# Performance work log

Hardware: AMD Instinct MI355X
Metric: run time of the kernel (lower is better)

The kernel has to match this reference:

```python
import jax, jax.numpy as jnp
import numpy as np

D_MODEL = 1024
N_HEADS = 16
D_K = D_MODEL // N_HEADS
D_FF = 4096
EPS = 1e-5


def _layernorm(x, g, b):
    mu = jnp.mean(x, axis=-1, keepdims=True)
    var = jnp.var(x, axis=-1, keepdims=True)
    return (x - mu) * jax.lax.rsqrt(var + EPS) * g + b


def setup_inputs() -> dict:
    key = jax.random.key(0)
    ks = jax.random.split(key, 12)
    s = 0.02
    x = jax.random.normal(ks[0], (2, 2048, D_MODEL), dtype=jnp.float32)
    # Linear weights stored [in, out] so y = x @ W + b
    wq = jax.random.normal(ks[1], (D_MODEL, D_MODEL), dtype=jnp.float32) * s
    wk = jax.random.normal(ks[2], (D_MODEL, D_MODEL), dtype=jnp.float32) * s
    wv = jax.random.normal(ks[3], (D_MODEL, D_MODEL), dtype=jnp.float32) * s
    wo = jax.random.normal(ks[4], (D_MODEL, D_MODEL), dtype=jnp.float32) * s
    bq = jnp.zeros((D_MODEL,), jnp.float32)
    bk = jnp.zeros((D_MODEL,), jnp.float32)
    bv = jnp.zeros((D_MODEL,), jnp.float32)
    bo = jnp.zeros((D_MODEL,), jnp.float32)
    ln1_g = jnp.ones((D_MODEL,), jnp.float32)
    ln1_b = jnp.zeros((D_MODEL,), jnp.float32)
    ln2_g = jnp.ones((D_MODEL,), jnp.float32)
    ln2_b = jnp.zeros((D_MODEL,), jnp.float32)
    w1 = jax.random.normal(ks[5], (D_MODEL, D_FF), dtype=jnp.float32) * s
    b1 = jnp.zeros((D_FF,), jnp.float32)
    w2 = jax.random.normal(ks[6], (D_FF, D_MODEL), dtype=jnp.float32) * s
    b2 = jnp.zeros((D_MODEL,), jnp.float32)
    return {"x": x, "wq": wq, "bq": bq, "wk": wk, "bk": bk, "wv": wv, "bv": bv,
            "wo": wo, "bo": bo, "ln1_g": ln1_g, "ln1_b": ln1_b,
            "ln2_g": ln2_g, "ln2_b": ln2_b, "w1": w1, "b1": b1, "w2": w2, "b2": b2}


def reference(x, wq, bq, wk, bk, wv, bv, wo, bo, ln1_g, ln1_b, ln2_g, ln2_b, w1, b1, w2, b2):
    B, S, _ = x.shape
    res = x
    # project and split heads: [B, S, H, Dk]
    q = (x @ wq + bq).reshape(B, S, N_HEADS, D_K)
    k = (x @ wk + bk).reshape(B, S, N_HEADS, D_K)
    v = (x @ wv + bv).reshape(B, S, N_HEADS, D_K)
    # full score matrix [B, H, Sq, Sk] (faithful to unfused original)
    scores = jnp.einsum('bqhd,bkhd->bhqk', q, k) / jnp.sqrt(jnp.float32(D_K))
    weights = jax.nn.softmax(scores, axis=-1)
    attn = jnp.einsum('bhqk,bkhd->bqhd', weights, v).reshape(B, S, D_MODEL)
    x = _layernorm(res + attn @ wo + bo, ln1_g, ln1_b)
    res = x
    h = jax.nn.relu(x @ w1 + b1)
    x = _layernorm(res + h @ w2 + b2, ln2_g, ln2_b)
    return x
```

## Files before the change

kernel.cpp:

```cpp
#include <hip/hip_runtime.h>
#include <hip/hip_bf16.h>
#include <stdint.h>


typedef __hip_bfloat16 bf16;
typedef short bf16x8 __attribute__((ext_vector_type(8)));
typedef float f32x4 __attribute__((ext_vector_type(4)));

#if __has_builtin(__builtin_amdgcn_exp2f)
#define EXP2F(x) __builtin_amdgcn_exp2f(x)
#else
#define EXP2F(x) exp2f(x)
#endif

__device__ __forceinline__ float bf2f_lo(unsigned u) { return __uint_as_float(u << 16); }
__device__ __forceinline__ float bf2f_hi(unsigned u) { return __uint_as_float(u & 0xffff0000u); }
__device__ __forceinline__ ushort f2bf(float f) {
  union { bf16 h; ushort u; } c; c.h = __float2bfloat16(f); return c.u;
}
__device__ __forceinline__ uint pk_bf16(float a, float b) {
  union { __hip_bfloat162 h2; uint u; } c;
  c.h2 = __float22bfloat162_rn(make_float2(a, b));
  return c.u;
}
__device__ __forceinline__ bool is_f32(const uint* probe) { return probe[0] == 0x3F800000u; }
__device__ __forceinline__ float ld_param(const void* p, size_t i, bool f32) {
  return f32 ? ((const float*)p)[i] : __bfloat162float(((const bf16*)p)[i]);
}

__device__ __forceinline__ void barrier_raw() {
  asm volatile("" ::: "memory");
  __builtin_amdgcn_s_barrier();
  asm volatile("" ::: "memory");
}
__device__ __forceinline__ void lgkm0() {
  asm volatile("s_waitcnt lgkmcnt(0)" ::: "memory");
}
__device__ __forceinline__ void glds16(const ushort* g, ushort* l) {
  __builtin_amdgcn_global_load_lds(
      (const __attribute__((address_space(1))) void*)g,
      (__attribute__((address_space(3))) void*)l, 16, 0, 0);
}

#define MFMA16(MH, NH)                                                        \
  do {                                                                        \
    _Pragma("unroll") for (int c_ = 0; c_ < 2; ++c_)                          \
    _Pragma("unroll") for (int fi_ = 0; fi_ < 4; ++fi_)                       \
    _Pragma("unroll") for (int gi_ = 0; gi_ < 2; ++gi_)                       \
      acc[(MH) * 4 + fi_][(NH) * 2 + gi_] =                                   \
          __builtin_amdgcn_mfma_f32_16x16x32_bf16(                            \
              areg[fi_][c_], breg[(NH) * 2 + gi_][c_],                        \
              acc[(MH) * 4 + fi_][(NH) * 2 + gi_], 0, 0, 0);                  \
  } while (0)

__device__ __forceinline__ void gemm256_body(
    const ushort* __restrict__ A, const ushort* __restrict__ BT,
    const void* __restrict__ bias, const void* __restrict__ res,
    void* __restrict__ C, int N_, int K_, int bm, int bn,
    int kb, int ke, int mode, const uint* probe) {
  __shared__ ushort As[2][16384];
  __shared__ ushort Bs[2][16384];

  const int tid = threadIdx.x;
  const int wave = tid >> 6;
  const int lane = tid & 63;
  const int wm = wave >> 2;
  const int wn = wave & 3;
  const int m16 = lane & 15;
  const int quad = lane >> 4;
  const int nt = (ke - kb) >> 6;

  const int srow = lane >> 2;
  const int skc = ((lane & 3) * 8) ^ (((lane >> 5) & 1) << 4);
  const ushort* pA = A + (size_t)(bm * 256 + wave * 16 + srow) * K_ + kb + skc;
  const ushort* pB = BT + (size_t)(bn * 256 + wave * 16 + srow) * K_ + kb + skc;
  const size_t hstep = (size_t)128 * K_;
  ushort* dA = &As[0][0] + wave * 1024;
  ushort* dB = &Bs[0][0] + wave * 1024;

  auto stageA = [&](int b, int half, int t) {
    const ushort* g = pA + (size_t)half * hstep + t * 64;
    ushort* d = dA + b * 16384 + half * 8192;
    glds16(g, d);
    glds16(g + 32, d + 512);
  };
  auto stageB = [&](int b, int half, int t) {
    const ushort* g = pB + (size_t)half * hstep + t * 64;
    ushort* d = dB + b * 16384 + half * 8192;
    glds16(g, d);
    glds16(g + 32, d + 512);
  };

  const int fr_off = m16 * 32 + ((quad * 8) ^ (((m16 >> 3) & 1) << 4));
  const ushort* rA = &As[0][0] + fr_off;
  const ushort* rB = &Bs[0][0] + fr_off;
  auto ldA = [&](int b, int f, int c) {
    return *(const bf16x8*)(rA + b * 16384 +
                            ((f >> 2) * 8 + wm * 4 + (f & 3)) * 1024 + c * 512);
  };
  auto ldB = [&](int b, int g, int c) {
    return *(const bf16x8*)(rB + b * 16384 +
                            ((g >> 1) * 8 + wn * 2 + (g & 1)) * 1024 + c * 512);
  };

  f32x4 acc[8][4];
#pragma unroll
  for (int f = 0; f < 8; ++f)
#pragma unroll
    for (int g = 0; g < 4; ++g) acc[f][g] = (f32x4){0.f, 0.f, 0.f, 0.f};
  bf16x8 areg[4][2], breg[4][2];

  stageA(0, 0, 0); stageB(0, 0, 0); stageA(0, 1, 0); stageB(0, 1, 0);
  if (nt > 1) { stageA(1, 0, 1); stageB(1, 0, 1); }
  asm volatile("s_waitcnt vmcnt(4)" ::: "memory");
  barrier_raw();

  for (int t = 0; t < nt; ++t) {
    const int b = t & 1, bo = b ^ 1;
#pragma unroll
    for (int fi = 0; fi < 4; ++fi) { areg[fi][0] = ldA(b, fi, 0); areg[fi][1] = ldA(b, fi, 1); }
#pragma unroll
    for (int gi = 0; gi < 2; ++gi) { breg[gi][0] = ldB(b, gi, 0); breg[gi][1] = ldB(b, gi, 1); }
    if (t + 1 < nt) stageA(bo, 1, t + 1);
    barrier_raw(); lgkm0();
    __builtin_amdgcn_s_setprio(1); MFMA16(0, 0); __builtin_amdgcn_s_setprio(0);
    barrier_raw();
#pragma unroll
    for (int gi = 2; gi < 4; ++gi) { breg[gi][0] = ldB(b, gi, 0); breg[gi][1] = ldB(b, gi, 1); }
    if (t + 1 < nt) stageB(bo, 1, t + 1);
    barrier_raw(); lgkm0();
    __builtin_amdgcn_s_setprio(1); MFMA16(0, 1); __builtin_amdgcn_s_setprio(0);
    barrier_raw();
#pragma unroll
    for (int fi = 0; fi < 4; ++fi) { areg[fi][0] = ldA(b, fi + 4, 0); areg[fi][1] = ldA(b, fi + 4, 1); }
    if (t + 2 < nt) stageA(b, 0, t + 2);
    barrier_raw(); lgkm0();
    __builtin_amdgcn_s_setprio(1); MFMA16(1, 0); __builtin_amdgcn_s_setprio(0);
    barrier_raw();
    if (t + 2 < nt) stageB(b, 0, t + 2);
    barrier_raw(); lgkm0();
    __builtin_amdgcn_s_setprio(1); MFMA16(1, 1); __builtin_amdgcn_s_setprio(0);
    if (t + 2 < nt) asm volatile("s_waitcnt vmcnt(4)" ::: "memory");
    else            asm volatile("s_waitcnt vmcnt(0)" ::: "memory");
    barrier_raw();
  }

  const bool F32 = is_f32(probe);
#pragma unroll
  for (int g = 0; g < 4; ++g) {
    const int col = bn * 256 + (g >> 1) * 128 + wn * 32 + (g & 1) * 16 + m16;
    const float bv = (mode >= 3) ? 0.f : ld_param(bias, col, F32);
#pragma unroll
    for (int f = 0; f < 8; ++f) {
      const int rowb = bm * 256 + (f >> 2) * 128 + wm * 64 + (f & 3) * 16 + quad * 4;
#pragma unroll
      for (int r = 0; r < 4; ++r) {
        const int row = rowb + r;
        float v = acc[f][g][r] + bv;
        if (mode == 1) v = fmaxf(v, 0.f);
        if (mode == 2) v += __bfloat162float(((const bf16*)res)[(size_t)row * N_ + col]);
        if (mode == 2 || mode == 3) ((float*)C)[(size_t)row * N_ + col] = v;
        else ((bf16*)C)[(size_t)row * N_ + col] = __float2bfloat16(v);
      }
    }
  }
}

__global__ __launch_bounds__(512, 2) void gemm256_qkv(
    const ushort* A, const ushort* BT0, const ushort* BT1, const ushort* BT2,
    const void* b0, const void* b1, const void* b2,
    bf16* C0, bf16* C1, bf16* C2, const uint* probe) {
  const int sel = blockIdx.y >> 2, bn = blockIdx.y & 3;
  const ushort* BT = sel == 0 ? BT0 : (sel == 1 ? BT1 : BT2);
  const void* bb = sel == 0 ? b0 : (sel == 1 ? b1 : b2);
  bf16* C = sel == 0 ? C0 : (sel == 1 ? C1 : C2);
  gemm256_body(A, BT, bb, nullptr, C, 1024, 1024, blockIdx.x, bn, 0, 1024, 0, probe);
}
__global__ __launch_bounds__(512, 2) void gemm256_ffn1(
    const ushort* A, const ushort* BT, const void* bias, bf16* C, const uint* probe) {
  gemm256_body(A, BT, bias, nullptr, C, 4096, 1024,
               blockIdx.x, blockIdx.y, 0, 1024, 1, probe);
}
__global__ __launch_bounds__(512, 2) void gemm256_ffn2_sk4(
    const ushort* A, const ushort* BT,
    bf16* P0, bf16* P1, bf16* P2, bf16* P3, const uint* probe) {
  const int kz = blockIdx.z;
  bf16* C = kz == 0 ? P0 : kz == 1 ? P1 : kz == 2 ? P2 : P3;
  gemm256_body(A, BT, nullptr, nullptr, C, 1024, 4096, blockIdx.x, blockIdx.y,
               kz * 1024, kz * 1024 + 1024, 4, probe);
}

template <bool A_EXT, bool RES_EXT>
__device__ __forceinline__ void gemm_body(
    const void* __restrict__ Av, const ushort* __restrict__ BT,
    const void* __restrict__ bias, const void* __restrict__ res,
    void* __restrict__ C, int N_, int K_, int bm, int bn,
    int kb, int ke, int mode, const uint* probe) {
  __shared__ ushort Asm_[128 * 32];
  __shared__ ushort Bsm_[128 * 32];

  const bool F32 = is_f32(probe);
  const bool AF = A_EXT && F32;

  const int tid = threadIdx.x;
  const int wave = tid >> 6;
  const int lane = tid & 63;
  const int wm = wave & 1, wn = wave >> 1;

  const int r0 = tid >> 2;
  const int c0 = (tid & 3) * 8;
  const int dA0 = r0 * 32 + c0;
  const int dA1 = dA0 + 64 * 32;

  const size_t aRow0 = (size_t)(bm * 128 + r0) * K_;
  const size_t aRow1 = aRow0 + (size_t)64 * K_;
  const ushort* pB0 = BT + (size_t)(bn * 128 + r0) * K_ + c0;
  const ushort* pB1 = pB0 + (size_t)64 * K_;

  auto ld4 = [&](int kk, uint4& A0, uint4& A1, uint4& B0, uint4& B1) {
    if (AF) {
      const float* Af = (const float*)Av;
      const float4 f0 = *(const float4*)(Af + aRow0 + kk + c0);
      const float4 f1 = *(const float4*)(Af + aRow0 + kk + c0 + 4);
      const float4 g0 = *(const float4*)(Af + aRow1 + kk + c0);
      const float4 g1 = *(const float4*)(Af + aRow1 + kk + c0 + 4);
      A0.x = pk_bf16(f0.x, f0.y); A0.y = pk_bf16(f0.z, f0.w);
      A0.z = pk_bf16(f1.x, f1.y); A0.w = pk_bf16(f1.z, f1.w);
      A1.x = pk_bf16(g0.x, g0.y); A1.y = pk_bf16(g0.z, g0.w);
      A1.z = pk_bf16(g1.x, g1.y); A1.w = pk_bf16(g1.z, g1.w);
    } else {
      const ushort* Ab = (const ushort*)Av;
      A0 = *(const uint4*)(Ab + aRow0 + kk + c0);
      A1 = *(const uint4*)(Ab + aRow1 + kk + c0);
    }
    B0 = *(const uint4*)(pB0 + kk);
    B1 = *(const uint4*)(pB1 + kk);
  };

  f32x4 zero = {0.f, 0.f, 0.f, 0.f};
  f32x4 acc[4][4];
#pragma unroll
  for (int i = 0; i < 4; ++i)
#pragma unroll
    for (int j = 0; j < 4; ++j) acc[i][j] = zero;

  const int m16 = lane & 15;
  const int quad = lane >> 4;
  const int koff = quad * 8;

  uint4 a0, a1, b0, b1;
  ld4(kb, a0, a1, b0, b1);

  for (int k0 = kb; k0 < ke; k0 += 32) {
    __syncthreads();
    *(uint4*)&Asm_[dA0] = a0;
    *(uint4*)&Asm_[dA1] = a1;
    *(uint4*)&Bsm_[dA0] = b0;
    *(uint4*)&Bsm_[dA1] = b1;
    __syncthreads();

    if (k0 + 32 < ke) ld4(k0 + 32, a0, a1, b0, b1);

    bf16x8 af[4], bfr[4];
#pragma unroll
    for (int i = 0; i < 4; ++i)
      af[i] = *(const bf16x8*)&Asm_[(wm * 64 + i * 16 + m16) * 32 + koff];
#pragma unroll
    for (int j = 0; j < 4; ++j)
      bfr[j] = *(const bf16x8*)&Bsm_[(wn * 64 + j * 16 + m16) * 32 + koff];
#pragma unroll
    for (int i = 0; i < 4; ++i)
#pragma unroll
      for (int j = 0; j < 4; ++j)
        acc[i][j] = __builtin_amdgcn_mfma_f32_16x16x32_bf16(af[i], bfr[j], acc[i][j], 0, 0, 0);
  }

  const int row0 = bm * 128 + wm * 64;
  const int col0 = bn * 128 + wn * 64;
#pragma unroll
  for (int j = 0; j < 4; ++j) {
    const int col = col0 + j * 16 + m16;
    const float bv = (mode == 3) ? 0.f : ld_param(bias, col, F32);
#pragma unroll
    for (int i = 0; i < 4; ++i) {
#pragma unroll
      for (int r = 0; r < 4; ++r) {
        const int row = row0 + i * 16 + quad * 4 + r;
        float v = acc[i][j][r] + bv;
        if (mode == 1) v = fmaxf(v, 0.f);
        if (mode == 2) v += ld_param(res, (size_t)row * N_ + col, RES_EXT && F32);
        if (mode >= 2) ((float*)C)[(size_t)row * N_ + col] = v;
        else ((bf16*)C)[(size_t)row * N_ + col] = __float2bfloat16(v);
      }
    }
  }
}

__global__ __launch_bounds__(256) void gemm_wo_sk(
    const ushort* A, const ushort* BT, const void* bias, const void* res,
    float* C0, float* C1, const uint* probe) {
  const int kz = blockIdx.z;
  gemm_body<false, true>(A, BT, bias, res, kz ? C1 : C0, 1024, 1024,
                         blockIdx.x, blockIdx.y, kz * 512, kz * 512 + 512,
                         kz ? 3 : 2, probe);
}

__global__ __launch_bounds__(256) void transpose_all(
    const void* W0, const void* W1, const void* W2, const void* W3,
    const void* W4, const void* W5, const void* X6,
    ushort* D0, ushort* D1, ushort* D2, ushort* D3, ushort* D4, ushort* D5,
    ushort* D6, const uint* probe) {
  const int z = blockIdx.z;
  if (z == 6) {
    const bool F32 = is_f32(probe);
    const size_t i =
        ((size_t)(blockIdx.y * 128 + blockIdx.x) * 256 + threadIdx.x) * 4;
    if (F32) {
      const float4 a = *(const float4*)((const float*)X6 + i);
      uint2 o; o.x = pk_bf16(a.x, a.y); o.y = pk_bf16(a.z, a.w);
      *(uint2*)(D6 + i) = o;
    } else {
      *(uint2*)(D6 + i) = *(const uint2*)((const ushort*)X6 + i);
    }
    return;
  }
  if (z < 4 && blockIdx.x >= 32) return;
  int n0, k0, K_, N_;
  const void* W;
  ushort* D;
  if (z < 4) {
    n0 = blockIdx.x * 32; k0 = blockIdx.y * 32; K_ = 1024; N_ = 1024;
    W = z == 0 ? W0 : z == 1 ? W1 : z == 2 ? W2 : W3;
    D = z == 0 ? D0 : z == 1 ? D1 : z == 2 ? D2 : D3;
  } else if (z == 4) {
    n0 = blockIdx.x * 32; k0 = blockIdx.y * 32; K_ = 1024; N_ = 4096; W = W4; D = D4;
  } else {
    n0 = blockIdx.y * 32; k0 = blockIdx.x * 32; K_ = 4096; N_ = 1024; W = W5; D = D5;
  }
  const bool F32 = is_f32(probe);
  __shared__ ushort tile[32][33];
  const int tx = threadIdx.x & 31, ty = threadIdx.x >> 5;
#pragma unroll
  for (int i = 0; i < 32; i += 8) {
    const size_t src = (size_t)(k0 + ty + i) * N_ + n0 + tx;
    tile[ty + i][tx] = F32 ? f2bf(((const float*)W)[src]) : ((const ushort*)W)[src];
  }
  __syncthreads();
#pragma unroll
  for (int i = 0; i < 32; i += 8)
    D[(size_t)(n0 + ty + i) * K_ + k0 + tx] = tile[tx][ty + i];
}

template <bool OUT_EXT>
__global__ __launch_bounds__(256) void ln_kernel(
    const float* __restrict__ X, const float* __restrict__ P,
    const void* __restrict__ g, const void* __restrict__ bta,
    void* __restrict__ out, const uint* probe) {
  const bool F32 = is_f32(probe);
  const int row = blockIdx.x;
  const int tid = threadIdx.x;
  const float4 a = *(const float4*)(X + (size_t)row * 1024 + tid * 4);
  const float4 b = *(const float4*)(P + (size_t)row * 1024 + tid * 4);
  const float xv[4] = {a.x + b.x, a.y + b.y, a.z + b.z, a.w + b.w};
  float s = xv[0] + xv[1] + xv[2] + xv[3];
  float ss = xv[0] * xv[0] + xv[1] * xv[1] + xv[2] * xv[2] + xv[3] * xv[3];
#pragma unroll
  for (int o = 32; o > 0; o >>= 1) { s += __shfl_down(s, o); ss += __shfl_down(ss, o); }
  __shared__ float red[8];
  if ((tid & 63) == 0) { red[tid >> 6] = s; red[4 + (tid >> 6)] = ss; }
  __syncthreads();
  s = red[0] + red[1] + red[2] + red[3];
  ss = red[4] + red[5] + red[6] + red[7];
  const float mu = s * (1.f / 1024.f);
  const float rstd = rsqrtf(ss * (1.f / 1024.f) - mu * mu + 1e-5f);
#pragma unroll
  for (int i = 0; i < 4; ++i) {
    const size_t idx = (size_t)row * 1024 + tid * 4 + i;
    const float y = (xv[i] - mu) * rstd * ld_param(g, tid * 4 + i, F32) +
                    ld_param(bta, tid * 4 + i, F32);
    if (OUT_EXT && F32) ((float*)out)[idx] = y;
    else ((bf16*)out)[idx] = __float2bfloat16(y);
  }
}

template <bool OUT_EXT>
__global__ __launch_bounds__(256) void ln4_kernel(
    const ushort* __restrict__ P0, const ushort* __restrict__ P1,
    const ushort* __restrict__ P2, const ushort* __restrict__ P3,
    const ushort* __restrict__ resX, const void* __restrict__ b2,
    const void* __restrict__ g, const void* __restrict__ bta,
    void* __restrict__ out, const uint* probe) {
  const bool F32 = is_f32(probe);
  const int row = blockIdx.x;
  const int tid = threadIdx.x;
  const size_t base = (size_t)row * 1024 + tid * 4;
  float xv[4];
  {
    const uint2 ur = *(const uint2*)(resX + base);
    xv[0] = bf2f_lo(ur.x) + ld_param(b2, tid * 4 + 0, F32);
    xv[1] = bf2f_hi(ur.x) + ld_param(b2, tid * 4 + 1, F32);
    xv[2] = bf2f_lo(ur.y) + ld_param(b2, tid * 4 + 2, F32);
    xv[3] = bf2f_hi(ur.y) + ld_param(b2, tid * 4 + 3, F32);
  }
  auto addv = [&](const ushort* P) {
    const uint2 u = *(const uint2*)(P + base);
    xv[0] += bf2f_lo(u.x); xv[1] += bf2f_hi(u.x);
    xv[2] += bf2f_lo(u.y); xv[3] += bf2f_hi(u.y);
  };
  addv(P0); addv(P1); addv(P2); addv(P3);
  float s = xv[0] + xv[1] + xv[2] + xv[3];
  float ss = xv[0] * xv[0] + xv[1] * xv[1] + xv[2] * xv[2] + xv[3] * xv[3];
#pragma unroll
  for (int o = 32; o > 0; o >>= 1) { s += __shfl_down(s, o); ss += __shfl_down(ss, o); }
  __shared__ float red[8];
  if ((tid & 63) == 0) { red[tid >> 6] = s; red[4 + (tid >> 6)] = ss; }
  __syncthreads();
  s = red[0] + red[1] + red[2] + red[3];
  ss = red[4] + red[5] + red[6] + red[7];
  const float mu = s * (1.f / 1024.f);
  const float rstd = rsqrtf(ss * (1.f / 1024.f) - mu * mu + 1e-5f);
#pragma unroll
  for (int i = 0; i < 4; ++i) {
    const size_t idx = base + i;
    const float y = (xv[i] - mu) * rstd * ld_param(g, tid * 4 + i, F32) +
                    ld_param(bta, tid * 4 + i, F32);
    if (OUT_EXT && F32) ((float*)out)[idx] = y;
    else ((bf16*)out)[idx] = __float2bfloat16(y);
  }
}

__global__ __launch_bounds__(256, 4) void attn_mfma(
    const ushort* __restrict__ Qm, const ushort* __restrict__ Km,
    const ushort* __restrict__ Vm, ushort* __restrict__ Om) {
  __shared__ ushort Ks[2][4096];
  __shared__ ushort Vt[4096];
  __shared__ ushort Pw[4][1024];

  const int tid = threadIdx.x;
  const int wave = tid >> 6, lane = tid & 63;
  const int m16 = lane & 15, quad = lane >> 4;

  const int g = blockIdx.x;
  const int slot = g >> 3;
  const int bh = (g & 7) * 4 + (slot >> 5);
  const int qt = slot & 31;
  const int bb = bh >> 4, h = bh & 15;
  const size_t hb = ((size_t)bb * 2048) * 1024 + (size_t)h * 64;
  const int q0 = qt * 64 + wave * 16;

  const float QS = 0.125f * 1.44269504f;
  const int swz = (m16 >> 3) << 4;
  const int rdo = m16 * 32 + ((quad * 8) ^ swz);

  bf16x8 qf[2];
#pragma unroll
  for (int c = 0; c < 2; ++c) {
    const uint4 u = *(const uint4*)(Qm + hb + (size_t)(q0 + m16) * 1024 + c * 32 + quad * 8);
    const uint w[4] = {u.x, u.y, u.z, u.w};
    bf16x8 f;
#pragma unroll
    for (int j = 0; j < 4; ++j) {
      const uint p = pk_bf16(bf2f_lo(w[j]) * QS, bf2f_hi(w[j]) * QS);
      f[2 * j]     = (short)(p & 0xffffu);
      f[2 * j + 1] = (short)(p >> 16);
    }
    qf[c] = f;
  }

  f32x4 zero = {0.f, 0.f, 0.f, 0.f};
  f32x4 acc[4];
#pragma unroll
  for (int jd = 0; jd < 4; ++jd) acc[jd] = zero;
  float lp[4] = {0.f, 0.f, 0.f, 0.f};

  const int srow = lane >> 2;
  const int skc = ((lane & 3) * 8) ^ ((lane >> 5) << 4);
  const ushort* pK = Km + hb + (size_t)(wave * 16 + srow) * 1024 + skc;
  ushort* dK = &Ks[0][0] + wave * 1024;

  const int pp = tid & 31;
  const int dc = tid >> 5;
  const int ka_ = 16 * ((2 * pp) & 3) + ((2 * pp) >> 2);
  const int kb_ = 16 * ((2 * pp + 1) & 3) + ((2 * pp + 1) >> 2);
  const ushort* Vg = Vm + hb;
  const int vtb = (dc >> 1) * 1024 + (pp >> 4) * 512 + (dc & 1) * 256 +
                  ((2 * (pp & 15)) ^ ((dc & 1) << 4));

  glds16(pK, dK);
  glds16(pK + 32, dK + 512);
  uint4 vr0 = *(const uint4*)(Vg + (size_t)ka_ * 1024 + dc * 8);
  uint4 vr1 = *(const uint4*)(Vg + (size_t)kb_ * 1024 + dc * 8);
  asm volatile("s_waitcnt vmcnt(2)" ::: "memory");

  for (int kt = 0; kt < 2048; kt += 64) {
    const int b = (kt >> 6) & 1;
    __syncthreads();
    {
      const uint va[4] = {vr0.x, vr0.y, vr0.z, vr0.w};
      const uint vb[4] = {vr1.x, vr1.y, vr1.z, vr1.w};
#pragma unroll
      for (int j = 0; j < 8; ++j) {
        const uint lo = (j & 1) ? (va[j >> 1] >> 16) : (va[j >> 1] & 0xffffu);
        const uint hi = (j & 1) ? (vb[j >> 1] & 0xffff0000u) : (vb[j >> 1] << 16);
        *(uint*)&Vt[vtb + j * 32] = lo | hi;
      }
    }
    if (kt + 64 < 2048) {
      const ushort* gk = pK + (size_t)(kt + 64) * 1024;
      ushort* d = dK + (b ^ 1) * 4096;
      glds16(gk, d);
      glds16(gk + 32, d + 512);
    }
    __syncthreads();
    if (kt + 64 < 2048) {
      vr0 = *(const uint4*)(Vg + (size_t)(kt + 64 + ka_) * 1024 + dc * 8);
      vr1 = *(const uint4*)(Vg + (size_t)(kt + 64 + kb_) * 1024 + dc * 8);
    }

    f32x4 s[4];
#pragma unroll
    for (int jn = 0; jn < 4; ++jn) s[jn] = zero;
    __builtin_amdgcn_s_setprio(1);
#pragma unroll
    for (int c = 0; c < 2; ++c) {
      bf16x8 kb4[4];
#pragma unroll
      for (int jn = 0; jn < 4; ++jn)
        kb4[jn] = *(const bf16x8*)&Ks[b][jn * 1024 + c * 512 + rdo];
#pragma unroll
      for (int jn = 0; jn < 4; ++jn)
        s[jn] = __builtin_amdgcn_mfma_f32_16x16x32_bf16(qf[c], kb4[jn], s[jn], 0, 0, 0);
    }
    __builtin_amdgcn_s_setprio(0);

#pragma unroll
    for (int r = 0; r < 4; ++r) {
      const float p0 = EXP2F(s[0][r]);
      const float p1 = EXP2F(s[1][r]);
      const float p2 = EXP2F(s[2][r]);
      const float p3 = EXP2F(s[3][r]);
      lp[r] += (p0 + p1) + (p2 + p3);
      uint2 pk2;
      pk2.x = pk_bf16(p0, p1);
      pk2.y = pk_bf16(p2, p3);
      const int row = quad * 4 + r;
      *(uint2*)&Pw[wave][(m16 >> 3) * 512 + row * 32 +
                         (((m16 & 7) * 4) ^ ((row >> 3) << 4))] = pk2;
    }
    lgkm0();

    __builtin_amdgcn_s_setprio(1);
#pragma unroll
    for (int c = 0; c < 2; ++c) {
      bf16x8 vb4[4];
      const bf16x8 pa = *(const bf16x8*)&Pw[wave][c * 512 + rdo];
#pragma unroll
      for (int jd = 0; jd < 4; ++jd)
        vb4[jd] = *(const bf16x8*)&Vt[jd * 1024 + c * 512 + rdo];
#pragma unroll
      for (int jd = 0; jd < 4; ++jd)
        acc[jd] = __builtin_amdgcn_mfma_f32_16x16x32_bf16(pa, vb4[jd], acc[jd], 0, 0, 0);
    }
    __builtin_amdgcn_s_setprio(0);
    asm volatile("s_waitcnt vmcnt(2)" ::: "memory");
  }

#pragma unroll
  for (int r = 0; r < 4; ++r) {
    float l = lp[r];
    l += __shfl_xor(l, 1); l += __shfl_xor(l, 2);
    l += __shfl_xor(l, 4); l += __shfl_xor(l, 8);
    const float inv = 1.f / l;
    const size_t rowoff = hb + (size_t)(q0 + quad * 4 + r) * 1024;
#pragma unroll
    for (int jd = 0; jd < 4; ++jd)
      Om[rowoff + jd * 16 + m16] = f2bf(acc[jd][r] * inv);
  }
}

extern "C" void kernel_launch(void* const* d_in, const int* in_sizes, int n_in,
                              void* d_out, int out_size, void* d_ws, size_t ws_size,
                              hipStream_t stream) {
  const void* x   = d_in[0];
  const void* wq  = d_in[1];
  const void* bq  = d_in[2];
  const void* wk  = d_in[3];
  const void* bk  = d_in[4];
  const void* wv  = d_in[5];
  const void* bv  = d_in[6];
  const void* wo  = d_in[7];
  const void* bo  = d_in[8];
  const uint* probe = (const uint*)d_in[9];
  const void* ln1g = d_in[9];
  const void* ln1b = d_in[10];
  const void* ln2g = d_in[11];
  const void* ln2b = d_in[12];
  const void* w1  = d_in[13];
  const void* b1  = d_in[14];
  const void* w2  = d_in[15];
  const void* b2  = d_in[16];

  char* ws = (char*)d_ws;
  const size_t MB = 1ull << 20;
  ushort* wqT = (ushort*)(ws + 0 * MB);
  ushort* wkT = (ushort*)(ws + 2 * MB);
  ushort* wvT = (ushort*)(ws + 4 * MB);
  ushort* woT = (ushort*)(ws + 6 * MB);
  ushort* w1T = (ushort*)(ws + 8 * MB);
  ushort* w2T = (ushort*)(ws + 16 * MB);
  ushort* Qb  = (ushort*)(ws + 24 * MB);
  ushort* Kb  = (ushort*)(ws + 32 * MB);
  ushort* Vb  = (ushort*)(ws + 40 * MB);
  ushort* Xb  = (ushort*)(ws + 64 * MB);
  ushort* AO  = (ushort*)(ws + 72 * MB);
  float*  T1  = (float*)(ws + 24 * MB);
  float*  P1w = (float*)(ws + 40 * MB);
  ushort* X1  = (ushort*)(ws + 56 * MB);
  ushort* Hb  = (ushort*)(ws + 24 * MB);
  ushort* P2a = (ushort*)(ws + 0 * MB);
  ushort* P2b = (ushort*)(ws + 8 * MB);
  ushort* P2c = (ushort*)(ws + 64 * MB);
  ushort* P2d = (ushort*)(ws + 72 * MB);

  const dim3 blk(256);
  const dim3 blk512(512);
  transpose_all<<<dim3(128, 32, 7), blk, 0, stream>>>(
      wq, wk, wv, wo, w1, w2, x, wqT, wkT, wvT, woT, w1T, w2T, Xb, probe);

  gemm256_qkv<<<dim3(16, 12), blk512, 0, stream>>>(
      Xb, wqT, wkT, wvT, bq, bk, bv, (bf16*)Qb, (bf16*)Kb, (bf16*)Vb, probe);
  attn_mfma<<<dim3(1024), blk, 0, stream>>>(Qb, Kb, Vb, AO);
  gemm_wo_sk<<<dim3(32, 8, 2), blk, 0, stream>>>(AO, woT, bo, x, T1, P1w, probe);
  ln_kernel<false><<<dim3(4096), blk, 0, stream>>>(T1, P1w, ln1g, ln1b, X1, probe);
  gemm256_ffn1<<<dim3(16, 16), blk512, 0, stream>>>(X1, w1T, b1, (bf16*)Hb, probe);
  gemm256_ffn2_sk4<<<dim3(16, 4, 4), blk512, 0, stream>>>(
      Hb, w2T, (bf16*)P2a, (bf16*)P2b, (bf16*)P2c, (bf16*)P2d, probe);
  ln4_kernel<true><<<dim3(4096), blk, 0, stream>>>(
      P2a, P2b, P2c, P2d, X1, b2, ln2g, ln2b, d_out, probe);
}
```

Measured before the change: 354.7 us.

## Pre-transpose V in separate kernel and double-buffer V via direct LDS loads

```diff
diff --git a/kernel.cpp b/kernel.cpp
--- a/kernel.cpp
+++ b/kernel.cpp
@@ -349,6 +349,31 @@
 #pragma unroll
   for (int i = 0; i < 32; i += 8)
     D[(size_t)(n0 + ty + i) * K_ + k0 + tx] = tile[tx][ty + i];
+}
+
+__global__ __launch_bounds__(256) void transpose_v(
+    const ushort* __restrict__ Vb, ushort* __restrict__ VTp) {
+  __shared__ ushort t64[64][66];
+  const int tid = threadIdx.x;
+  const int ktb = blockIdx.x;
+  const int bh = blockIdx.y;
+  const int bb = bh >> 4, h = bh & 15;
+  const size_t hb = ((size_t)bb * 2048) * 1024 + (size_t)h * 64;
+  const int r = tid >> 2, c4 = (tid & 3) * 16;
+  const ushort* src = Vb + hb + (size_t)(ktb * 64 + r) * 1024 + c4;
+  *(uint4*)&t64[r][c4] = *(const uint4*)src;
+  *(uint4*)&t64[r][c4 + 8] = *(const uint4*)(src + 8);
+  __syncthreads();
+  ushort vals[16];
+#pragma unroll
+  for (int j = 0; j < 16; ++j) {
+    const int jj = c4 + j;
+    const int k = 16 * (jj & 3) + (jj >> 2);
+    vals[j] = t64[k][r];
+  }
+  ushort* dst = VTp + (size_t)bh * 131072 + (size_t)r * 2048 + ktb * 64 + c4;
+  *(uint4*)dst = *(uint4*)&vals[0];
+  *(uint4*)(dst + 8) = *(uint4*)&vals[8];
 }
 
 template <bool OUT_EXT>
@@ -431,9 +456,9 @@
 
 __global__ __launch_bounds__(256, 4) void attn_mfma(
     const ushort* __restrict__ Qm, const ushort* __restrict__ Km,
-    const ushort* __restrict__ Vm, ushort* __restrict__ Om) {
+    const ushort* __restrict__ VTp, ushort* __restrict__ Om) {
   __shared__ ushort Ks[2][4096];
-  __shared__ ushort Vt[4096];
+  __shared__ ushort Vs[2][4096];
   __shared__ ushort Pw[4][1024];
 
   const int tid = threadIdx.x;
@@ -446,6 +471,7 @@
   const int qt = slot & 31;
   const int bb = bh >> 4, h = bh & 15;
   const size_t hb = ((size_t)bb * 2048) * 1024 + (size_t)h * 64;
+  const size_t vo = (size_t)bh * 131072;
   const int q0 = qt * 64 + wave * 16;
 
   const float QS = 0.125f * 1.44269504f;
@@ -476,45 +502,28 @@
   const int srow = lane >> 2;
   const int skc = ((lane & 3) * 8) ^ ((lane >> 5) << 4);
   const ushort* pK = Km + hb + (size_t)(wave * 16 + srow) * 1024 + skc;
+  const ushort* pV = VTp + vo + (size_t)(wave * 16 + srow) * 2048 + skc;
   ushort* dK = &Ks[0][0] + wave * 1024;
-
-  const int pp = tid & 31;
-  const int dc = tid >> 5;
-  const int ka_ = 16 * ((2 * pp) & 3) + ((2 * pp) >> 2);
-  const int kb_ = 16 * ((2 * pp + 1) & 3) + ((2 * pp + 1) >> 2);
-  const ushort* Vg = Vm + hb;
-  const int vtb = (dc >> 1) * 1024 + (pp >> 4) * 512 + (dc & 1) * 256 +
-                  ((2 * (pp & 15)) ^ ((dc & 1) << 4));
+  ushort* dV = &Vs[0][0] + wave * 1024;
 
   glds16(pK, dK);
   glds16(pK + 32, dK + 512);
-  uint4 vr0 = *(const uint4*)(Vg + (size_t)ka_ * 1024 + dc * 8);
-  uint4 vr1 = *(const uint4*)(Vg + (size_t)kb_ * 1024 + dc * 8);
-  asm volatile("s_waitcnt vmcnt(2)" ::: "memory");
+  glds16(pV, dV);
+  glds16(pV + 32, dV + 512);
+  asm volatile("s_waitcnt vmcnt(0)" ::: "memory");
 
   for (int kt = 0; kt < 2048; kt += 64) {
     const int b = (kt >> 6) & 1;
     __syncthreads();
-    {
-      const uint va[4] = {vr0.x, vr0.y, vr0.z, vr0.w};
-      const uint vb[4] = {vr1.x, vr1.y, vr1.z, vr1.w};
-#pragma unroll
-      for (int j = 0; j < 8; ++j) {
-        const uint lo = (j & 1) ? (va[j >> 1] >> 16) : (va[j >> 1] & 0xffffu);
-        const uint hi = (j & 1) ? (vb[j >> 1] & 0xffff0000u) : (vb[j >> 1] << 16);
-        *(uint*)&Vt[vtb + j * 32] = lo | hi;
-      }
-    }
     if (kt + 64 < 2048) {
       const ushort* gk = pK + (size_t)(kt + 64) * 1024;
-      ushort* d = dK + (b ^ 1) * 4096;
-      glds16(gk, d);
-      glds16(gk + 32, d + 512);
-    }
-    __syncthreads();
-    if (kt + 64 < 2048) {
-      vr0 = *(const uint4*)(Vg + (size_t)(kt + 64 + ka_) * 1024 + dc * 8);
-      vr1 = *(const uint4*)(Vg + (size_t)(kt + 64 + kb_) * 1024 + dc * 8);
+      const ushort* gv = pV + (kt + 64);
+      ushort* dk2 = dK + (b ^ 1) * 4096;
+      ushort* dv2 = dV + (b ^ 1) * 4096;
+      glds16(gk, dk2);
+      glds16(gk + 32, dk2 + 512);
+      glds16(gv, dv2);
+      glds16(gv + 32, dv2 + 512);
     }
 
     f32x4 s[4];
@@ -556,13 +565,13 @@
       const bf16x8 pa = *(const bf16x8*)&Pw[wave][c * 512 + rdo];
 #pragma unroll
       for (int jd = 0; jd < 4; ++jd)
-        vb4[jd] = *(const bf16x8*)&Vt[jd * 1024 + c * 512 + rdo];
+        vb4[jd] = *(const bf16x8*)&Vs[b][jd * 1024 + c * 512 + rdo];
 #pragma unroll
       for (int jd = 0; jd < 4; ++jd)
         acc[jd] = __builtin_amdgcn_mfma_f32_16x16x32_bf16(pa, vb4[jd], acc[jd], 0, 0, 0);
     }
     __builtin_amdgcn_s_setprio(0);
-    asm volatile("s_waitcnt vmcnt(2)" ::: "memory");
+    asm volatile("s_waitcnt vmcnt(0)" ::: "memory");
   }
 
 #pragma unroll
@@ -611,6 +620,7 @@
   ushort* Qb  = (ushort*)(ws + 24 * MB);
   ushort* Kb  = (ushort*)(ws + 32 * MB);
   ushort* Vb  = (ushort*)(ws + 40 * MB);
+  ushort* VTp = (ushort*)(ws + 48 * MB);
   ushort* Xb  = (ushort*)(ws + 64 * MB);
   ushort* AO  = (ushort*)(ws + 72 * MB);
   float*  T1  = (float*)(ws + 24 * MB);
@@ -629,7 +639,8 @@
 
   gemm256_qkv<<<dim3(16, 12), blk512, 0, stream>>>(
       Xb, wqT, wkT, wvT, bq, bk, bv, (bf16*)Qb, (bf16*)Kb, (bf16*)Vb, probe);
-  attn_mfma<<<dim3(1024), blk, 0, stream>>>(Qb, Kb, Vb, AO);
+  transpose_v<<<dim3(32, 32), blk, 0, stream>>>(Vb, VTp);
+  attn_mfma<<<dim3(1024), blk, 0, stream>>>(Qb, Kb, VTp, AO);
   gemm_wo_sk<<<dim3(32, 8, 2), blk, 0, stream>>>(AO, woT, bo, x, T1, P1w, probe);
   ln_kernel<false><<<dim3(4096), blk, 0, stream>>>(T1, P1w, ln1g, ln1b, X1, probe);
   gemm256_ffn1<<<dim3(16, 16), blk512, 0, stream>>>(X1, w1T, b1, (bf16*)Hb, probe);
```

After: 360.2 us. About the same (+1.6%).
